# Performance work log

Measured on AMD Instinct MI355X. Metric: run time of the kernel, lower is better.

Reference implementation:

```python
import jax, jax.numpy as jnp
import numpy as np
import math

D = 768       # hidden_size
FF = 3072     # intermediate_size
H = 12        # num heads
L = 3         # decoder_num_hidden_layers
R = 4         # max_role_embeddings
CS = 512      # const_size
B = 256
C = 32
EPS = 1e-5


def _inorm(x):
    # InstanceNorm1d with affine=False on (N, C, L): normalize over last dim
    m = jnp.mean(x, axis=-1, keepdims=True)
    v = jnp.var(x, axis=-1, keepdims=True)
    return (x - m) * jax.lax.rsqrt(v + EPS)


def _mlp(x, w1, b1, w2, b2):
    h = jax.nn.gelu(x @ w1.T + b1, approximate=False)
    return h @ w2.T + b2


def _tree_layer(x, pe, iw, ib, ow, ob, w1, b1, w2, b2):
    # x: (N, 2, D); pe: (N, 2, D)
    qk_in = x + pe
    Wq, Wk, Wv = jnp.split(iw, 3, axis=0)
    bq, bk, bv = jnp.split(ib, 3)
    N = x.shape[0]
    hd = D // H
    q = (qk_in @ Wq.T + bq).reshape(N, 2, H, hd)
    k = (qk_in @ Wk.T + bk).reshape(N, 2, H, hd)
    v = (x @ Wv.T + bv).reshape(N, 2, H, hd)
    scores = jnp.einsum('nqhd,nkhd->nhqk', q, k) / math.sqrt(hd)
    a = jax.nn.softmax(scores, axis=-1)
    o = jnp.einsum('nhqk,nkhd->nqhd', a, v).reshape(N, 2, D)
    o = o @ ow.T + ob
    x = _inorm(x + o)
    f = jax.nn.gelu(x @ w1.T + b1, approximate=False) @ w2.T + b2
    x = _inorm(x + f)
    return x


def setup_inputs() -> dict:
    key = jax.random.key(0)
    ks = jax.random.split(key, 24)
    rn = lambda k, shape, s=0.02: jax.random.normal(k, shape, jnp.float32) * s
    inp = {
        'parent_ij': jax.random.normal(ks[0], (B, D), jnp.float32),
        'child_ikj': jax.random.normal(ks[1], (B, C, 2, D), jnp.float32),
        'parent_scores': jax.random.normal(ks[2], (B, 1), jnp.float32),
        'child_scores': jax.random.normal(ks[3], (B, C, 2), jnp.float32),
        'attn_in_w': rn(ks[4], (L, 3 * D, D)),
        'attn_in_b': rn(ks[5], (L, 3 * D)),
        'attn_out_w': rn(ks[6], (L, D, D)),
        'attn_out_b': rn(ks[7], (L, D)),
        'lin1_w': rn(ks[8], (L, FF, D)),
        'lin1_b': rn(ks[9], (L, FF)),
        'lin2_w': rn(ks[10], (L, D, FF)),
        'lin2_b': rn(ks[11], (L, D)),
        'pos_emb': rn(ks[12], (L, R, D)),
        'parent_w1': rn(ks[13], (D, D)), 'parent_b1': rn(ks[14], (D,)),
        'parent_w2': rn(ks[15], (CS, D)), 'parent_b2': rn(ks[16], (CS,)),
        'left_w1': rn(ks[17], (D, D)), 'left_b1': rn(ks[18], (D,)),
        'left_w2': rn(ks[19], (CS, D)), 'left_b2': rn(ks[20], (CS,)),
        'right_w1': rn(ks[21], (D, D)), 'right_b1': rn(ks[22], (D,)),
        'right_w2': rn(ks[23], (CS, D)), 'right_b2': rn(jax.random.fold_in(key, 99), (CS,)),
    }
    return inp


def reference(parent_ij, child_ikj, parent_scores, child_scores,
              attn_in_w, attn_in_b, attn_out_w, attn_out_b,
              lin1_w, lin1_b, lin2_w, lin2_b, pos_emb,
              parent_w1, parent_b1, parent_w2, parent_b2,
              left_w1, left_b1, left_w2, left_b2,
              right_w1, right_b1, right_w2, right_b2):
    b, c = child_ikj.shape[0], child_ikj.shape[1]
    N = b * c * 2
    # inputs: token0 = parent, token1 = flipped child; row parity 0 -> right child, 1 -> left child
    parent_ext = jnp.broadcast_to(parent_ij[:, None, None, :], (b, c, 2, D))
    child_flip = child_ikj[:, :, ::-1, :]
    x = jnp.stack([parent_ext, child_flip], axis=3).reshape(N, 2, D)

    # scoring heads (parent row is identical for even/odd rows)
    pc = _mlp(parent_ij, parent_w1, parent_b1, parent_w2, parent_b2)          # (b, CS)
    rc = _mlp(child_ikj[:, :, 1, :], right_w1, right_b1, right_w2, right_b2)  # (b, c, CS)
    lc = _mlp(child_ikj[:, :, 0, :], left_w1, left_b1, left_w2, left_b2)      # (b, c, CS)
    scale = 1.0 / math.sqrt(CS)
    left_score = jnp.einsum('bs,bcs->bc', pc, rc) * scale
    right_score = jnp.einsum('bs,bcs->bc', pc, lc) * scale
    outside_scores = jnp.stack([left_score, right_score], axis=2)  # (b, c, 2)

    role_ids = jnp.array([[0, 1], [0, 2]])  # (2, 2) roles for even/odd rows
    for l in range(L):
        pe = jnp.broadcast_to(pos_emb[l][role_ids][None], (b * c, 2, 2, D)).reshape(N, 2, D)
        x = _tree_layer(x, pe, attn_in_w[l], attn_in_b[l], attn_out_w[l], attn_out_b[l],
                        lin1_w[l], lin1_b[l], lin2_w[l], lin2_b[l])

    out_e_ij = _inorm(x.sum(axis=1)).reshape(b, c, 2, D)
    return outside_scores, out_e_ij
```

## Files before the change

### kernel.cpp

```cpp
#include <hip/hip_runtime.h>
#include <cstdint>
#include <cmath>

#define DD      768
#define FFD     3072
#define NH      12
#define HDIM    64
#define LAYERS  3
#define CSZ     512
#define NB      256
#define NC      32
#define NSEQ    (NB * NC * 2)
#define NTOK    (NSEQ * 2)

typedef unsigned short ushort_t;
using short8 = __attribute__((ext_vector_type(8))) short;
using f32x4  = __attribute__((ext_vector_type(4))) float;

static __device__ __forceinline__ float b2f(ushort_t u) {
    union { float f; uint32_t i; } x; x.i = ((uint32_t)u) << 16; return x.f;
}
static __device__ __forceinline__ ushort_t f2b(float f) {
    uint32_t i = __float_as_uint(f);
    uint32_t r = (i + 0x7fffu + ((i >> 16) & 1u)) >> 16;
    return (ushort_t)r;
}
static __device__ __forceinline__ float gelu_f(float x) {
    return 0.5f * x * (1.0f + erff(x * 0.70710678118654752f));
}
static __device__ __forceinline__ float wave_sum64(float v) {
#pragma unroll
    for (int off = 32; off > 0; off >>= 1) v += __shfl_xor(v, off, 64);
    return v;
}
static __device__ __forceinline__ void async_cp16(const void* g, void* l) {
    __builtin_amdgcn_global_load_lds((const __attribute__((address_space(1))) void*)g,
                                     (__attribute__((address_space(3))) void*)l, 16, 0, 0);
}
static __device__ __forceinline__ void wg_barrier() {
    asm volatile("" ::: "memory");
    __builtin_amdgcn_s_barrier();
    asm volatile("" ::: "memory");
}
#define WAITVM(N) asm volatile("s_waitcnt vmcnt(" #N ")" ::: "memory")
#define LDSFENCE() asm volatile("s_waitcnt lgkmcnt(0)" ::: "memory")

__global__ __launch_bounds__(256) void cvt_bf16(const float* __restrict__ s,
                                                ushort_t* __restrict__ d, int n) {
    const int i = (blockIdx.x * 256 + threadIdx.x) * 4;
    if (i < n) {
        const float4 v = *(const float4*)(s + i);
        ushort4 o;
        o.x = f2b(v.x); o.y = f2b(v.y); o.z = f2b(v.z); o.w = f2b(v.w);
        *(ushort4*)(d + i) = o;
    }
}

__global__ __launch_bounds__(192) void build_x(const float* __restrict__ parent,
                                               const float* __restrict__ child,
                                               ushort_t* __restrict__ X) {
    const int r = blockIdx.x;
    const int t = threadIdx.x;
    const int n = r >> 1, q = r & 1;
    const int i = n >> 6;
    const int k = (n >> 1) & 31;
    const int j = n & 1;
    const float* src = (q == 0) ? (parent + (size_t)i * DD)
                                : (child + ((size_t)((i * 32 + k) * 2 + (1 - j))) * DD);
    const float4 v = ((const float4*)src)[t];
    ushort4 o;
    o.x = f2b(v.x); o.y = f2b(v.y); o.z = f2b(v.z); o.w = f2b(v.w);
    ((ushort4*)(X + (size_t)r * DD))[t] = o;
}

__global__ __launch_bounds__(256) void gemm_bf16(const ushort_t* __restrict__ A, int lda,
                                                 const ushort_t* __restrict__ W,
                                                 const float* __restrict__ bias,
                                                 ushort_t* __restrict__ C, int ldc,
                                                 int K, int NT, int GM, int GN,
                                                 int dogelu) {
    __shared__ __align__(16) short smem[16384];
    short* As = smem;
    short* Bs = smem + 8192;

    const int st = blockIdx.x / (GM * GN);
    const int stn = NT / GN;
    const int srow = st / stn, scol = st - srow * stn;
    const int r = blockIdx.x - st * (GM * GN);
    const int mt = srow * GM + r / GN;
    const int nt = scol * GN + (r - (r / GN) * GN);
    const int m0 = mt * 128;
    const int n0 = nt * 128;

    const int tid = threadIdx.x;
    const int r0s = tid >> 2, c0s = (tid & 3) * 8;
    const ushort_t* Ag0 = A + (size_t)(m0 + r0s) * lda + c0s;
    const ushort_t* Ag1 = A + (size_t)(m0 + 64 + r0s) * lda + c0s;
    const ushort_t* Wg0 = W + (size_t)(n0 + r0s) * K + c0s;
    const ushort_t* Wg1 = W + (size_t)(n0 + 64 + r0s) * K + c0s;

    const int wid = tid >> 6, lane = tid & 63;
    const int wm = (wid >> 1) * 64, wn = (wid & 1) * 64;
    const int lm = lane & 15;
    const int ko = (lane >> 4) * 8;

    f32x4 acc[4][4];
#pragma unroll
    for (int i = 0; i < 4; ++i)
#pragma unroll
        for (int j = 0; j < 4; ++j) acc[i][j] = {0.f, 0.f, 0.f, 0.f};

    {
        async_cp16(Ag0, As + tid * 8);
        async_cp16(Ag1, As + 2048 + tid * 8);
        async_cp16(Wg0, Bs + tid * 8);
        async_cp16(Wg1, Bs + 2048 + tid * 8);
    }

    for (int k0 = 0; k0 < K; k0 += 32) {
        const int b = (k0 >> 5) & 1;
        const int boff = b * 4096;
        __syncthreads();
        if (k0 + 32 < K) {
            const int o = (boff ^ 4096);
            const int k = k0 + 32;
            async_cp16(Ag0 + k, As + o + tid * 8);
            async_cp16(Ag1 + k, As + o + 2048 + tid * 8);
            async_cp16(Wg0 + k, Bs + o + tid * 8);
            async_cp16(Wg1 + k, Bs + o + 2048 + tid * 8);
        }
        short8 af[4], bfr[4];
#pragma unroll
        for (int i = 0; i < 4; ++i)
            af[i] = *(const short8*)(As + boff + (wm + i * 16 + lm) * 32 + ko);
#pragma unroll
        for (int j = 0; j < 4; ++j)
            bfr[j] = *(const short8*)(Bs + boff + (wn + j * 16 + lm) * 32 + ko);
#pragma unroll
        for (int i = 0; i < 4; ++i)
#pragma unroll
            for (int j = 0; j < 4; ++j)
                acc[i][j] = __builtin_amdgcn_mfma_f32_16x16x32_bf16(af[i], bfr[j], acc[i][j], 0, 0, 0);
    }

    float* T = (float*)smem;
    float* Tw = T + wid * 1088;
    const int r4 = lane >> 4;
    const int rrow = lane >> 2;
    const int rc0 = (lane & 3) * 16;
    const int gcolb = n0 + wn;

    float4 bb[4];
    if (bias) {
#pragma unroll
        for (int t = 0; t < 4; ++t) bb[t] = *(const float4*)(bias + gcolb + rc0 + t * 4);
    } else {
#pragma unroll
        for (int t = 0; t < 4; ++t) bb[t] = make_float4(0.f, 0.f, 0.f, 0.f);
    }

#pragma unroll
    for (int i = 0; i < 4; ++i) {
        __syncthreads();
#pragma unroll
        for (int j = 0; j < 4; ++j)
#pragma unroll
            for (int rr = 0; rr < 4; ++rr)
                Tw[(r4 * 4 + rr) * 68 + j * 16 + lm] = acc[i][j][rr];
        __syncthreads();
        float o[16];
#pragma unroll
        for (int t = 0; t < 4; ++t)
            *(f32x4*)&o[t * 4] = *(const f32x4*)(Tw + rrow * 68 + rc0 + t * 4);
#pragma unroll
        for (int t = 0; t < 4; ++t) {
            o[t * 4 + 0] += ((const float*)&bb[t])[0];
            o[t * 4 + 1] += ((const float*)&bb[t])[1];
            o[t * 4 + 2] += ((const float*)&bb[t])[2];
            o[t * 4 + 3] += ((const float*)&bb[t])[3];
        }
        if (dogelu) {
#pragma unroll
            for (int t = 0; t < 16; ++t) o[t] = gelu_f(o[t]);
        }
        uint32_t pk[8];
#pragma unroll
        for (int t = 0; t < 8; ++t)
            pk[t] = (uint32_t)f2b(o[2 * t]) | ((uint32_t)f2b(o[2 * t + 1]) << 16);
        ushort_t* dst = C + (size_t)(m0 + wm + i * 16 + rrow) * ldc + gcolb + rc0;
        *(uint4*)dst = make_uint4(pk[0], pk[1], pk[2], pk[3]);
        *(uint4*)(dst + 8) = make_uint4(pk[4], pk[5], pk[6], pk[7]);
    }
}

__global__ __launch_bounds__(512, 2) void gemm256(const ushort_t* __restrict__ A, int lda,
                                                  const ushort_t* __restrict__ W,
                                                  const float* __restrict__ bias,
                                                  ushort_t* __restrict__ C, int ldc,
                                                  int K, int NT, int GM, int GN,
                                                  int dogelu) {
    __shared__ __align__(16) short smem[65536];
    const int tid = threadIdx.x;

    const int nwg = gridDim.x;
    const int bid = blockIdx.x;
    const int qx = nwg >> 3, rx = nwg & 7;
    const int xcd = bid & 7, pos = bid >> 3;
    const int wgid = (xcd < rx ? xcd * (qx + 1) : rx * (qx + 1) + (xcd - rx) * qx) + pos;
    const int stb = GM * GN;
    const int st = wgid / stb;
    const int stn = NT / GN;
    const int srow = st / stn, scol = st - srow * stn;
    const int r = wgid - st * stb;
    const int mt = srow * GM + r / GN;
    const int nt = scol * GN + (r - (r / GN) * GN);
    const int m0 = mt * 256, n0 = nt * 256;

    const int srow_t = tid >> 2;
    const int scol_t = ((tid & 3) ^ ((tid >> 3) & 3)) << 3;
    const ushort_t* Ag = A + (size_t)(m0 + srow_t) * lda + scol_t;
    const ushort_t* Bg = W + (size_t)(n0 + srow_t) * K + scol_t;
    short* ldsA = smem + tid * 8;
    short* ldsB = smem + 8192 + tid * 8;
    const size_t ldaH = (size_t)128 * lda;
    const size_t ldbH = (size_t)128 * K;

    auto stage = [&](int kt_) {
        const int b_ = (kt_ & 3) * 16384;
        const int k_ = kt_ * 32;
        async_cp16(Ag + k_,        ldsA + b_);
        async_cp16(Ag + ldaH + k_, ldsA + b_ + 4096);
        async_cp16(Bg + k_,        ldsB + b_);
        async_cp16(Bg + ldbH + k_, ldsB + b_ + 4096);
    };

    const int wid = tid >> 6, lane = tid & 63;
    const int wr = wid >> 2, wc = wid & 3;
    const int lm = lane & 15;
    const int swz = (((lane >> 4) ^ ((lane >> 1) & 3)) << 3);
    const short* rdA = smem + (wr * 128 + lm) * 32 + swz;
    const short* rdB = smem + 8192 + (wc * 64 + lm) * 32 + swz;

    f32x4 acc[8][4];
#pragma unroll
    for (int i = 0; i < 8; ++i)
#pragma unroll
        for (int j = 0; j < 4; ++j) acc[i][j] = {0.f, 0.f, 0.f, 0.f};

    const int NKT = K >> 5;
    stage(0); stage(1); stage(2);

    for (int kt = 0; kt < NKT; ++kt) {
        if (kt + 3 < NKT)      { stage(kt + 3); WAITVM(12); }
        else if (kt + 2 < NKT) { WAITVM(8); }
        else if (kt + 1 < NKT) { WAITVM(4); }
        else                   { WAITVM(0); }
        wg_barrier();
        const int boff = (kt & 3) * 16384;
        short8 af[8], bfr[4];
#pragma unroll
        for (int i = 0; i < 8; ++i) af[i] = *(const short8*)(rdA + boff + i * 512);
#pragma unroll
        for (int j = 0; j < 4; ++j) bfr[j] = *(const short8*)(rdB + boff + j * 512);
        __builtin_amdgcn_s_setprio(1);
#pragma unroll
        for (int i = 0; i < 8; ++i)
#pragma unroll
            for (int j = 0; j < 4; ++j)
                acc[i][j] = __builtin_amdgcn_mfma_f32_16x16x32_bf16(af[i], bfr[j], acc[i][j], 0, 0, 0);
        __builtin_amdgcn_s_setprio(0);
        wg_barrier();
    }

    float* T = (float*)smem;
    float* Tw = T + wid * 1088;
    const int r4 = lane >> 4;
    const int rrow = lane >> 2;
    const int rc0 = (lane & 3) * 16;
    const int gcolb = n0 + wc * 64;

    float4 bb[4];
#pragma unroll
    for (int t = 0; t < 4; ++t) bb[t] = *(const float4*)(bias + gcolb + rc0 + t * 4);

#pragma unroll
    for (int mi = 0; mi < 8; ++mi) {
#pragma unroll
        for (int j = 0; j < 4; ++j)
#pragma unroll
            for (int rr = 0; rr < 4; ++rr)
                Tw[(r4 * 4 + rr) * 68 + j * 16 + lm] = acc[mi][j][rr];
        LDSFENCE();
        float o[16];
#pragma unroll
        for (int t = 0; t < 4; ++t)
            *(f32x4*)&o[t * 4] = *(const f32x4*)(Tw + rrow * 68 + rc0 + t * 4);
#pragma unroll
        for (int t = 0; t < 4; ++t) {
            o[t * 4 + 0] += ((const float*)&bb[t])[0];
            o[t * 4 + 1] += ((const float*)&bb[t])[1];
            o[t * 4 + 2] += ((const float*)&bb[t])[2];
            o[t * 4 + 3] += ((const float*)&bb[t])[3];
        }
        if (dogelu) {
#pragma unroll
            for (int t = 0; t < 16; ++t) o[t] = gelu_f(o[t]);
        }
        uint32_t pk[8];
#pragma unroll
        for (int t = 0; t < 8; ++t)
            pk[t] = (uint32_t)f2b(o[2 * t]) | ((uint32_t)f2b(o[2 * t + 1]) << 16);
        ushort_t* dst = C + (size_t)(m0 + wr * 128 + mi * 16 + rrow) * ldc + gcolb + rc0;
        *(uint4*)dst = make_uint4(pk[0], pk[1], pk[2], pk[3]);
        *(uint4*)(dst + 8) = make_uint4(pk[4], pk[5], pk[6], pk[7]);
        LDSFENCE();
    }
}

__global__ __launch_bounds__(256) void pe_proj(const float* __restrict__ pel,
                                               const float* __restrict__ aiwl,
                                               float* __restrict__ PEQ,
                                               float* __restrict__ PEK) {
    const int wid = threadIdx.x >> 6, lane = threadIdx.x & 63;
    const int task = blockIdx.x * 4 + wid;
    const int which = task >= 3 * DD;
    const int idx = task - which * 3 * DD;
    const int r = idx / DD, o = idx - r * DD;
    const float* pe = pel + (size_t)r * DD;
    const float* w = aiwl + (size_t)(which ? DD + o : o) * DD;
    float s = 0.f;
#pragma unroll
    for (int e = 0; e < 12; ++e) s += pe[e * 64 + lane] * w[e * 64 + lane];
    s = wave_sum64(s);
    if (lane == 0) (which ? PEK : PEQ)[r * DD + o] = s;
}

__global__ __launch_bounds__(256) void attn_kernel(const ushort_t* __restrict__ QKV,
                                                   const float* __restrict__ peq,
                                                   const float* __restrict__ pek,
                                                   ushort_t* __restrict__ O,
                                                   int seq0) {
    const int wid = threadIdx.x >> 6;
    const int lane = threadIdx.x & 63;
    const int task = blockIdx.x * 4 + wid;
    const int ns = task / NH;
    const int h = task - ns * NH;
    const int j = (seq0 + ns) & 1;
    const ushort_t* base = QKV + (size_t)(2 * ns) * (3 * DD);
    const int c = h * HDIM + lane;
    const int role1 = (1 + j) * DD;

    const float q0 = b2f(base[c]) + peq[c];
    const float k0 = b2f(base[DD + c]) + pek[c];
    const float v0 = b2f(base[2 * DD + c]);
    const ushort_t* base1 = base + 3 * DD;
    const float q1 = b2f(base1[c]) + peq[role1 + c];
    const float k1 = b2f(base1[DD + c]) + pek[role1 + c];
    const float v1 = b2f(base1[2 * DD + c]);

    float p00 = q0 * k0, p01 = q0 * k1, p10 = q1 * k0, p11 = q1 * k1;
#pragma unroll
    for (int off = 32; off > 0; off >>= 1) {
        p00 += __shfl_xor(p00, off, 64);
        p01 += __shfl_xor(p01, off, 64);
        p10 += __shfl_xor(p10, off, 64);
        p11 += __shfl_xor(p11, off, 64);
    }
    const float sc = 0.125f;
    const float s00 = p00 * sc, s01 = p01 * sc, s10 = p10 * sc, s11 = p11 * sc;

    const float m0 = fmaxf(s00, s01);
    const float e00 = __expf(s00 - m0), e01 = __expf(s01 - m0);
    const float a00 = e00 / (e00 + e01);
    const float o0 = a00 * v0 + (1.0f - a00) * v1;

    const float m1 = fmaxf(s10, s11);
    const float e10 = __expf(s10 - m1), e11 = __expf(s11 - m1);
    const float a10 = e10 / (e10 + e11);
    const float o1 = a10 * v0 + (1.0f - a10) * v1;

    O[(size_t)(2 * ns) * DD + c] = f2b(o0);
    O[(size_t)(2 * ns + 1) * DD + c] = f2b(o1);
}

__global__ __launch_bounds__(256) void add_inorm(ushort_t* __restrict__ x,
                                                 const ushort_t* __restrict__ d) {
    const int wid = threadIdx.x >> 6, lane = threadIdx.x & 63;
    const int r = blockIdx.x * 4 + wid;
    ushort_t* xr = x + (size_t)r * DD;
    const ushort_t* dr = d + (size_t)r * DD;
    float v[12];
    float s = 0.f, ss = 0.f;
#pragma unroll
    for (int e = 0; e < 3; ++e) {
        const ushort4 xa = ((const ushort4*)xr)[e * 64 + lane];
        const ushort4 da = ((const ushort4*)dr)[e * 64 + lane];
        const float a0 = b2f(xa.x) + b2f(da.x);
        const float a1 = b2f(xa.y) + b2f(da.y);
        const float a2 = b2f(xa.z) + b2f(da.z);
        const float a3 = b2f(xa.w) + b2f(da.w);
        v[e * 4 + 0] = a0; v[e * 4 + 1] = a1; v[e * 4 + 2] = a2; v[e * 4 + 3] = a3;
        s += a0 + a1 + a2 + a3;
        ss += a0 * a0 + a1 * a1 + a2 * a2 + a3 * a3;
    }
    s = wave_sum64(s); ss = wave_sum64(ss);
    const float mean = s * (1.0f / DD);
    const float var = ss * (1.0f / DD) - mean * mean;
    const float rs = rsqrtf(var + 1e-5f);
#pragma unroll
    for (int e = 0; e < 3; ++e) {
        ushort4 o;
        o.x = f2b((v[e * 4 + 0] - mean) * rs);
        o.y = f2b((v[e * 4 + 1] - mean) * rs);
        o.z = f2b((v[e * 4 + 2] - mean) * rs);
        o.w = f2b((v[e * 4 + 3] - mean) * rs);
        ((ushort4*)xr)[e * 64 + lane] = o;
    }
}

__global__ __launch_bounds__(256) void final_inorm(const ushort_t* __restrict__ x,
                                                   float* __restrict__ out) {
    const int wid = threadIdx.x >> 6, lane = threadIdx.x & 63;
    const int n = blockIdx.x * 4 + wid;
    const ushort_t* r0 = x + (size_t)(2 * n) * DD;
    const ushort_t* r1 = r0 + DD;
    float v[12];
    float s = 0.f, ss = 0.f;
#pragma unroll
    for (int e = 0; e < 3; ++e) {
        const ushort4 xa = ((const ushort4*)r0)[e * 64 + lane];
        const ushort4 xb = ((const ushort4*)r1)[e * 64 + lane];
        const float a0 = b2f(xa.x) + b2f(xb.x);
        const float a1 = b2f(xa.y) + b2f(xb.y);
        const float a2 = b2f(xa.z) + b2f(xb.z);
        const float a3 = b2f(xa.w) + b2f(xb.w);
        v[e * 4 + 0] = a0; v[e * 4 + 1] = a1; v[e * 4 + 2] = a2; v[e * 4 + 3] = a3;
        s += a0 + a1 + a2 + a3;
        ss += a0 * a0 + a1 * a1 + a2 * a2 + a3 * a3;
    }
    s = wave_sum64(s); ss = wave_sum64(ss);
    const float mean = s * (1.0f / DD);
    const float var = ss * (1.0f / DD) - mean * mean;
    const float rs = rsqrtf(var + 1e-5f);
    float* orow = out + (size_t)n * DD;
#pragma unroll
    for (int e = 0; e < 3; ++e) {
        float4 o;
        o.x = (v[e * 4 + 0] - mean) * rs;
        o.y = (v[e * 4 + 1] - mean) * rs;
        o.z = (v[e * 4 + 2] - mean) * rs;
        o.w = (v[e * 4 + 3] - mean) * rs;
        ((float4*)orow)[e * 64 + lane] = o;
    }
}

__global__ __launch_bounds__(256) void score_dot(const ushort_t* __restrict__ pc,
                                                 const ushort_t* __restrict__ cc,
                                                 float* __restrict__ out, int which) {
    const int wid = threadIdx.x >> 6;
    const int lane = threadIdx.x & 63;
    const int row = blockIdx.x * 4 + wid;
    const int b = row >> 5;
    const ushort_t* p = pc + (size_t)b * CSZ;
    const ushort_t* c = cc + (size_t)row * CSZ;
    float s = 0.f;
#pragma unroll
    for (int e = 0; e < 8; ++e) s += b2f(p[e * 64 + lane]) * b2f(c[e * 64 + lane]);
    s = wave_sum64(s);
    if (lane == 0) out[row * 2 + which] = s * 0.04419417382415922f;
}

extern "C" void kernel_launch(void* const* d_in, const int* in_sizes, int n_in,
                              void* d_out, int out_size, void* d_ws, size_t ws_size,
                              hipStream_t stream) {
    const float* parent = (const float*)d_in[0];
    const float* child  = (const float*)d_in[1];
    const float* aiw = (const float*)d_in[4];
    const float* aib = (const float*)d_in[5];
    const float* aow = (const float*)d_in[6];
    const float* aob = (const float*)d_in[7];
    const float* l1w = (const float*)d_in[8];
    const float* l1b = (const float*)d_in[9];
    const float* l2w = (const float*)d_in[10];
    const float* l2b = (const float*)d_in[11];
    const float* pemb = (const float*)d_in[12];
    const float* pw1 = (const float*)d_in[13];
    const float* pb1 = (const float*)d_in[14];
    const float* pw2 = (const float*)d_in[15];
    const float* pb2 = (const float*)d_in[16];
    const float* lw1 = (const float*)d_in[17];
    const float* lb1 = (const float*)d_in[18];
    const float* lw2 = (const float*)d_in[19];
    const float* lb2 = (const float*)d_in[20];
    const float* rw1 = (const float*)d_in[21];
    const float* rb1 = (const float*)d_in[22];
    const float* rw2 = (const float*)d_in[23];
    const float* rb2 = (const float*)d_in[24];
    float* out = (float*)d_out;
    (void)in_sizes; (void)n_in; (void)out_size;

    int CH = 8192;
    {
        const size_t fixedB = 100ull * 1024 * 1024;
        if (ws_size >= fixedB + (size_t)32768 * 4608 * 2) CH = 32768;
        else if (ws_size >= fixedB + (size_t)16384 * 4608 * 2) CH = 16384;
    }
    const int NCH = NTOK / CH;

    ushort_t* W0 = (ushort_t*)d_ws;
    size_t off = 0;
    auto take = [&](size_t elems) { ushort_t* p = W0 + off; off += (elems + 127) & ~(size_t)127; return p; };
    ushort_t* aiw_b = take((size_t)LAYERS * 3 * DD * DD);
    ushort_t* aow_b = take((size_t)LAYERS * DD * DD);
    ushort_t* l1w_b = take((size_t)LAYERS * FFD * DD);
    ushort_t* l2w_b = take((size_t)LAYERS * DD * FFD);
    ushort_t* pw1_b = take((size_t)DD * DD);
    ushort_t* pw2_b = take((size_t)CSZ * DD);
    ushort_t* lw1_b = take((size_t)DD * DD);
    ushort_t* lw2_b = take((size_t)CSZ * DD);
    ushort_t* rw1_b = take((size_t)DD * DD);
    ushort_t* rw2_b = take((size_t)CSZ * DD);
    ushort_t* Pb    = take((size_t)NB * DD);
    ushort_t* Xb    = take((size_t)NTOK * DD);
    ushort_t* S1b   = take((size_t)CH * FFD);
    ushort_t* S2b   = take((size_t)CH * DD);
    ushort_t* S3b   = take((size_t)CH * DD);
    ushort_t* P1b   = take((size_t)NB * DD);
    ushort_t* P2b   = take((size_t)NB * CSZ);
    float* PEQ = (float*)(W0 + off); off += 2 * 3 * DD;
    float* PEK = PEQ + 3 * DD;

    auto cvt = [&](const float* s, ushort_t* d, size_t n) {
        cvt_bf16<<<(int)((n + 1023) / 1024), 256, 0, stream>>>(s, d, (int)n);
    };
    auto gemm = [&](const ushort_t* A, int lda, const ushort_t* Wt, const float* bias,
                    ushort_t* C, int ldc, int M, int N, int K, int dg) {
        if (M % 256 == 0 && N % 256 == 0 && M >= 8192 && N >= 768 && K % 32 == 0) {
            const int MT = M / 256, NT = N / 256;
            const int GM = (MT % 8 == 0) ? 8 : ((MT % 4 == 0) ? 4 : MT);
            int GN = 8;
            while (NT % GN) --GN;
            gemm256<<<MT * NT, 512, 0, stream>>>(A, lda, Wt, bias, C, ldc, K, NT, GM, GN, dg);
        } else {
            const int MT = M / 128, NT = N / 128;
            const int GM = (MT % 8 == 0) ? 8 : MT;
            int GN = 8;
            while (NT % GN) --GN;
            gemm_bf16<<<MT * NT, 256, 0, stream>>>(A, lda, Wt, bias, C, ldc, K, NT, GM, GN, dg);
        }
    };

    cvt(aiw, aiw_b, (size_t)LAYERS * 3 * DD * DD);
    cvt(aow, aow_b, (size_t)LAYERS * DD * DD);
    cvt(l1w, l1w_b, (size_t)LAYERS * FFD * DD);
    cvt(l2w, l2w_b, (size_t)LAYERS * DD * FFD);
    cvt(pw1, pw1_b, (size_t)DD * DD);
    cvt(pw2, pw2_b, (size_t)CSZ * DD);
    cvt(lw1, lw1_b, (size_t)DD * DD);
    cvt(lw2, lw2_b, (size_t)CSZ * DD);
    cvt(rw1, rw1_b, (size_t)DD * DD);
    cvt(rw2, rw2_b, (size_t)CSZ * DD);
    cvt(parent, Pb, (size_t)NB * DD);
    cvt(child, S1b, (size_t)NB * NC * 2 * DD);

    build_x<<<NTOK, 192, 0, stream>>>(parent, child, Xb);

    gemm(Pb, DD, pw1_b, pb1, P1b, DD, NB, DD, DD, 1);
    gemm(P1b, DD, pw2_b, pb2, P2b, CSZ, NB, CSZ, DD, 0);
    gemm(S1b, 2 * DD, lw1_b, lb1, S2b, DD, NB * NC, DD, DD, 1);
    gemm(S2b, DD, lw2_b, lb2, S3b, CSZ, NB * NC, CSZ, DD, 0);
    score_dot<<<NB * NC / 4, 256, 0, stream>>>(P2b, S3b, out, 1);
    gemm(S1b + DD, 2 * DD, rw1_b, rb1, S2b, DD, NB * NC, DD, DD, 1);
    gemm(S2b, DD, rw2_b, rb2, S3b, CSZ, NB * NC, CSZ, DD, 0);
    score_dot<<<NB * NC / 4, 256, 0, stream>>>(P2b, S3b, out, 0);

    for (int l = 0; l < LAYERS; ++l) {
        const ushort_t* Wl  = aiw_b + (size_t)l * 3 * DD * DD;
        const float* bl  = aib + (size_t)l * 3 * DD;
        const ushort_t* owl = aow_b + (size_t)l * DD * DD;
        const float* obl = aob + (size_t)l * DD;
        const ushort_t* w1l = l1w_b + (size_t)l * FFD * DD;
        const float* b1l = l1b + (size_t)l * FFD;
        const ushort_t* w2l = l2w_b + (size_t)l * DD * FFD;
        const float* b2l = l2b + (size_t)l * DD;

        pe_proj<<<2 * 3 * DD / 4, 256, 0, stream>>>(pemb + (size_t)l * 4 * DD,
                                                    aiw + (size_t)l * 3 * DD * DD, PEQ, PEK);

        for (int c = 0; c < NCH; ++c) {
            ushort_t* Xc = Xb + (size_t)c * CH * DD;
            gemm(Xc, DD, Wl, bl, S1b, 3 * DD, CH, 3 * DD, DD, 0);
            attn_kernel<<<(CH / 2) * NH / 4, 256, 0, stream>>>(S1b, PEQ, PEK, S2b, c * (CH / 2));
            gemm(S2b, DD, owl, obl, S3b, DD, CH, DD, DD, 0);
            add_inorm<<<CH / 4, 256, 0, stream>>>(Xc, S3b);
            gemm(Xc, DD, w1l, b1l, S1b, FFD, CH, FFD, DD, 1);
            gemm(S1b, FFD, w2l, b2l, S3b, DD, CH, DD, FFD, 0);
            add_inorm<<<CH / 4, 256, 0, stream>>>(Xc, S3b);
        }
    }

    final_inorm<<<NSEQ / 4, 256, 0, stream>>>(Xb, out + NSEQ);
}
```

Baseline: 2.721 ms.

## Split gemm256 k-step into two half phases interleaving LDS reads, copies and MFMAs

Each k-iteration of the 256x256 GEMM main loop is split into two halves. The first half issues the A-tile async copy for a future stage and runs MFMAs on the first four A fragments. The second half loads the remaining A fragments, issues the B-tile copy, and runs the other MFMAs. The goal is to overlap global-to-LDS copies and LDS fragment reads with matrix-core work, and to shorten the fragment register footprint. The cost is four workgroup barriers per k-step instead of two. A K>=96 guard keeps the three-stage prologue valid.

```diff
diff --git a/kernel.cpp b/kernel.cpp
--- a/kernel.cpp
+++ b/kernel.cpp
@@ -225,11 +225,15 @@
     const size_t ldaH = (size_t)128 * lda;
     const size_t ldbH = (size_t)128 * K;
 
-    auto stage = [&](int kt_) {
+    auto stage2A = [&](int kt_) {
         const int b_ = (kt_ & 3) * 16384;
         const int k_ = kt_ * 32;
         async_cp16(Ag + k_,        ldsA + b_);
         async_cp16(Ag + ldaH + k_, ldsA + b_ + 4096);
+    };
+    auto stage2B = [&](int kt_) {
+        const int b_ = (kt_ & 3) * 16384;
+        const int k_ = kt_ * 32;
         async_cp16(Bg + k_,        ldsB + b_);
         async_cp16(Bg + ldbH + k_, ldsB + b_ + 4096);
     };
@@ -248,26 +252,42 @@
         for (int j = 0; j < 4; ++j) acc[i][j] = {0.f, 0.f, 0.f, 0.f};
 
     const int NKT = K >> 5;
-    stage(0); stage(1); stage(2);
+    stage2A(0); stage2B(0); stage2A(1); stage2B(1); stage2A(2); stage2B(2);
+    WAITVM(8);
+    wg_barrier();
 
     for (int kt = 0; kt < NKT; ++kt) {
-        if (kt + 3 < NKT)      { stage(kt + 3); WAITVM(12); }
-        else if (kt + 2 < NKT) { WAITVM(8); }
-        else if (kt + 1 < NKT) { WAITVM(4); }
+        const int boff = (kt & 3) * 16384;
+        short8 af[4], bfr[4], ag[4];
+#pragma unroll
+        for (int j = 0; j < 4; ++j) bfr[j] = *(const short8*)(rdB + boff + j * 512);
+#pragma unroll
+        for (int i = 0; i < 4; ++i) af[i] = *(const short8*)(rdA + boff + i * 512);
+        if (kt + 3 < NKT) stage2A(kt + 3);
+        wg_barrier();
+        LDSFENCE();
+        __builtin_amdgcn_s_setprio(1);
+#pragma unroll
+        for (int i = 0; i < 4; ++i)
+#pragma unroll
+            for (int j = 0; j < 4; ++j)
+                acc[i][j] = __builtin_amdgcn_mfma_f32_16x16x32_bf16(af[i], bfr[j], acc[i][j], 0, 0, 0);
+        __builtin_amdgcn_s_setprio(0);
+        wg_barrier();
+#pragma unroll
+        for (int i = 0; i < 4; ++i) ag[i] = *(const short8*)(rdA + boff + (4 + i) * 512);
+        if (kt + 3 < NKT) stage2B(kt + 3);
+        if (kt + 3 < NKT)      { WAITVM(8); }
+        else if (kt + 2 < NKT) { WAITVM(4); }
         else                   { WAITVM(0); }
         wg_barrier();
-        const int boff = (kt & 3) * 16384;
-        short8 af[8], bfr[4];
-#pragma unroll
-        for (int i = 0; i < 8; ++i) af[i] = *(const short8*)(rdA + boff + i * 512);
-#pragma unroll
-        for (int j = 0; j < 4; ++j) bfr[j] = *(const short8*)(rdB + boff + j * 512);
+        LDSFENCE();
         __builtin_amdgcn_s_setprio(1);
 #pragma unroll
-        for (int i = 0; i < 8; ++i)
+        for (int i = 0; i < 4; ++i)
 #pragma unroll
             for (int j = 0; j < 4; ++j)
-                acc[i][j] = __builtin_amdgcn_mfma_f32_16x16x32_bf16(af[i], bfr[j], acc[i][j], 0, 0, 0);
+                acc[4 + i][j] = __builtin_amdgcn_mfma_f32_16x16x32_bf16(ag[i], bfr[j], acc[4 + i][j], 0, 0, 0);
         __builtin_amdgcn_s_setprio(0);
         wg_barrier();
     }
@@ -535,7 +555,7 @@
     };
     auto gemm = [&](const ushort_t* A, int lda, const ushort_t* Wt, const float* bias,
                     ushort_t* C, int ldc, int M, int N, int K, int dg) {
-        if (M % 256 == 0 && N % 256 == 0 && M >= 8192 && N >= 768 && K % 32 == 0) {
+        if (M % 256 == 0 && N % 256 == 0 && M >= 8192 && N >= 768 && K >= 96 && K % 32 == 0) {
             const int MT = M / 256, NT = N / 256;
             const int GM = (MT % 8 == 0) ? 8 : ((MT % 4 == 0) ? 4 : MT);
             int GN = 8;
```

New measurement: 2.587 ms. 1.05x faster.

## Replace 256x256 GEMM with 128x256 tile, double-buffered, higher occupancy

Applied to the files above, without the earlier changes.

Swaps the large-shape GEMM kernel for a 128x256 output tile per workgroup. It uses a 2-stage double buffer in place of the 4-stage LDS pipeline, cutting shared memory from 128KB to 48KB so up to four workgroups fit per CU. Each wave accumulates 4x4 MFMA tiles instead of 8x4. The aim is better occupancy and lower register/LDS pressure, at the cost of less data reuse per tile and a shallower prefetch that waits on all outstanding loads every step.

```diff
diff --git a/kernel.cpp b/kernel.cpp
--- a/kernel.cpp
+++ b/kernel.cpp
@@ -193,13 +193,13 @@
     }
 }
 
-__global__ __launch_bounds__(512, 2) void gemm256(const ushort_t* __restrict__ A, int lda,
-                                                  const ushort_t* __restrict__ W,
-                                                  const float* __restrict__ bias,
-                                                  ushort_t* __restrict__ C, int ldc,
-                                                  int K, int NT, int GM, int GN,
-                                                  int dogelu) {
-    __shared__ __align__(16) short smem[65536];
+__global__ __launch_bounds__(512, 4) void gemm_mid(const ushort_t* __restrict__ A, int lda,
+                                                   const ushort_t* __restrict__ W,
+                                                   const float* __restrict__ bias,
+                                                   ushort_t* __restrict__ C, int ldc,
+                                                   int K, int NT, int GM, int GN,
+                                                   int dogelu) {
+    __shared__ __align__(16) short smem[24576];
     const int tid = threadIdx.x;
 
     const int nwg = gridDim.x;
@@ -214,22 +214,20 @@
     const int r = wgid - st * stb;
     const int mt = srow * GM + r / GN;
     const int nt = scol * GN + (r - (r / GN) * GN);
-    const int m0 = mt * 256, n0 = nt * 256;
+    const int m0 = mt * 128, n0 = nt * 256;
 
     const int srow_t = tid >> 2;
     const int scol_t = ((tid & 3) ^ ((tid >> 3) & 3)) << 3;
     const ushort_t* Ag = A + (size_t)(m0 + srow_t) * lda + scol_t;
     const ushort_t* Bg = W + (size_t)(n0 + srow_t) * K + scol_t;
+    const size_t ldbH = (size_t)128 * K;
     short* ldsA = smem + tid * 8;
-    short* ldsB = smem + 8192 + tid * 8;
-    const size_t ldaH = (size_t)128 * lda;
-    const size_t ldbH = (size_t)128 * K;
-
-    auto stage = [&](int kt_) {
-        const int b_ = (kt_ & 3) * 16384;
-        const int k_ = kt_ * 32;
+    short* ldsB = smem + 4096 + tid * 8;
+
+    auto stage = [&](int s_) {
+        const int b_ = (s_ & 1) * 12288;
+        const int k_ = s_ * 32;
         async_cp16(Ag + k_,        ldsA + b_);
-        async_cp16(Ag + ldaH + k_, ldsA + b_ + 4096);
         async_cp16(Bg + k_,        ldsB + b_);
         async_cp16(Bg + ldbH + k_, ldsB + b_ + 4096);
     };
@@ -238,42 +236,36 @@
     const int wr = wid >> 2, wc = wid & 3;
     const int lm = lane & 15;
     const int swz = (((lane >> 4) ^ ((lane >> 1) & 3)) << 3);
-    const short* rdA = smem + (wr * 128 + lm) * 32 + swz;
-    const short* rdB = smem + 8192 + (wc * 64 + lm) * 32 + swz;
-
-    f32x4 acc[8][4];
-#pragma unroll
-    for (int i = 0; i < 8; ++i)
+    const short* rdA0 = smem + (wr * 64 + lm) * 32 + swz;
+    const short* rdB0 = smem + 4096 + (wc * 64 + lm) * 32 + swz;
+
+    f32x4 acc[4][4];
+#pragma unroll
+    for (int i = 0; i < 4; ++i)
 #pragma unroll
         for (int j = 0; j < 4; ++j) acc[i][j] = {0.f, 0.f, 0.f, 0.f};
 
-    const int NKT = K >> 5;
-    stage(0); stage(1); stage(2);
-
-    for (int kt = 0; kt < NKT; ++kt) {
-        if (kt + 3 < NKT)      { stage(kt + 3); WAITVM(12); }
-        else if (kt + 2 < NKT) { WAITVM(8); }
-        else if (kt + 1 < NKT) { WAITVM(4); }
-        else                   { WAITVM(0); }
+    const int NS = K >> 5;
+    stage(0);
+    for (int s = 0; s < NS; ++s) {
+        const int boff = (s & 1) * 12288;
+        WAITVM(0);
         wg_barrier();
-        const int boff = (kt & 3) * 16384;
-        short8 af[8], bfr[4];
-#pragma unroll
-        for (int i = 0; i < 8; ++i) af[i] = *(const short8*)(rdA + boff + i * 512);
-#pragma unroll
-        for (int j = 0; j < 4; ++j) bfr[j] = *(const short8*)(rdB + boff + j * 512);
-        __builtin_amdgcn_s_setprio(1);
-#pragma unroll
-        for (int i = 0; i < 8; ++i)
+        if (s + 1 < NS) stage(s + 1);
+        short8 af[4], bf[4];
+#pragma unroll
+        for (int i = 0; i < 4; ++i) af[i] = *(const short8*)(rdA0 + boff + i * 512);
+#pragma unroll
+        for (int j = 0; j < 4; ++j) bf[j] = *(const short8*)(rdB0 + boff + j * 512);
+#pragma unroll
+        for (int i = 0; i < 4; ++i)
 #pragma unroll
             for (int j = 0; j < 4; ++j)
-                acc[i][j] = __builtin_amdgcn_mfma_f32_16x16x32_bf16(af[i], bfr[j], acc[i][j], 0, 0, 0);
-        __builtin_amdgcn_s_setprio(0);
-        wg_barrier();
-    }
-
-    float* T = (float*)smem;
-    float* Tw = T + wid * 1088;
+                acc[i][j] = __builtin_amdgcn_mfma_f32_16x16x32_bf16(af[i], bf[j], acc[i][j], 0, 0, 0);
+    }
+    wg_barrier();
+
+    float* Tw = (float*)smem + wid * 1088;
     const int r4 = lane >> 4;
     const int rrow = lane >> 2;
     const int rc0 = (lane & 3) * 16;
@@ -284,7 +276,7 @@
     for (int t = 0; t < 4; ++t) bb[t] = *(const float4*)(bias + gcolb + rc0 + t * 4);
 
 #pragma unroll
-    for (int mi = 0; mi < 8; ++mi) {
+    for (int mi = 0; mi < 4; ++mi) {
 #pragma unroll
         for (int j = 0; j < 4; ++j)
 #pragma unroll
@@ -310,7 +302,7 @@
 #pragma unroll
         for (int t = 0; t < 8; ++t)
             pk[t] = (uint32_t)f2b(o[2 * t]) | ((uint32_t)f2b(o[2 * t + 1]) << 16);
-        ushort_t* dst = C + (size_t)(m0 + wr * 128 + mi * 16 + rrow) * ldc + gcolb + rc0;
+        ushort_t* dst = C + (size_t)(m0 + wr * 64 + mi * 16 + rrow) * ldc + gcolb + rc0;
         *(uint4*)dst = make_uint4(pk[0], pk[1], pk[2], pk[3]);
         *(uint4*)(dst + 8) = make_uint4(pk[4], pk[5], pk[6], pk[7]);
         LDSFENCE();
@@ -535,12 +527,12 @@
     };
     auto gemm = [&](const ushort_t* A, int lda, const ushort_t* Wt, const float* bias,
                     ushort_t* C, int ldc, int M, int N, int K, int dg) {
-        if (M % 256 == 0 && N % 256 == 0 && M >= 8192 && N >= 768 && K % 32 == 0) {
-            const int MT = M / 256, NT = N / 256;
+        if (M % 128 == 0 && N % 256 == 0 && M >= 8192 && N >= 768 && K % 32 == 0) {
+            const int MT = M / 128, NT = N / 256;
             const int GM = (MT % 8 == 0) ? 8 : ((MT % 4 == 0) ? 4 : MT);
             int GN = 8;
             while (NT % GN) --GN;
-            gemm256<<<MT * NT, 512, 0, stream>>>(A, lda, Wt, bias, C, ldc, K, NT, GM, GN, dg);
+            gemm_mid<<<MT * NT, 512, 0, stream>>>(A, lda, Wt, bias, C, ldc, K, NT, GM, GN, dg);
         } else {
             const int MT = M / 128, NT = N / 128;
             const int GM = (MT % 8 == 0) ? 8 : MT;
```

Result: faster. 2.462 ms (-9.5%).
